# Kernel tuning notes

Measured on AMD Instinct MI355X. Metric: run time of the kernel, lower is better.

The kernel has to match this reference:

```python
import jax, jax.numpy as jnp
import numpy as np

L, N, E, NODE_D, EDGE_D, H = 3, 50000, 800000, 64, 16, 128
EPS = 1e-5


def _ln(x, g, b):
    mu = jnp.mean(x, axis=-1, keepdims=True)
    var = jnp.var(x, axis=-1, keepdims=True)
    return (x - mu) * jax.lax.rsqrt(var + EPS) * g + b


def setup_inputs() -> dict:
    key = jax.random.key(0)
    ks = jax.random.split(key, 16)
    inp = {
        "x": jax.random.normal(ks[0], (N, NODE_D), dtype=jnp.float32),
        "edge_index": jax.random.randint(ks[1], (2, E), 0, N, dtype=jnp.int64 if jax.config.jax_enable_x64 else jnp.int32),
        "edge_attr": jax.random.normal(ks[2], (E, EDGE_D), dtype=jnp.float32),
        # node_embed: Linear(node_dim, H) + LayerNorm
        "node_W": jax.random.normal(ks[3], (H, NODE_D), dtype=jnp.float32) * (2.0 / H) ** 0.5,
        "node_b": jnp.zeros((H,), jnp.float32),
        "node_ln_g": jnp.ones((H,), jnp.float32),
        "node_ln_b": jnp.zeros((H,), jnp.float32),
        # per-layer GINConv params, stacked on leading layer dim
        "edge_W": jax.random.normal(ks[4], (L, H, EDGE_D), dtype=jnp.float32) * (2.0 / H) ** 0.5,
        "edge_b": jnp.zeros((L, H), jnp.float32),
        "edge_ln_g": jnp.ones((L, H), jnp.float32),
        "edge_ln_b": jnp.zeros((L, H), jnp.float32),
        "sl_attr": jax.random.normal(ks[5], (L, 1, EDGE_D), dtype=jnp.float32),
        "mlp_W1": jax.random.normal(ks[6], (L, 2 * H, H), dtype=jnp.float32) * (1.0 / H) ** 0.5,
        "mlp_b1": jnp.zeros((L, 2 * H), jnp.float32),
        "mlp_W2": jax.random.normal(ks[7], (L, H, 2 * H), dtype=jnp.float32) * (1.0 / (2 * H)) ** 0.5,
        "mlp_b2": jnp.zeros((L, H), jnp.float32),
        # BatchNorm1d affine params (batch-stat / training-mode math)
        "bn_g": jnp.ones((L, H), jnp.float32),
        "bn_b": jnp.zeros((L, H), jnp.float32),
    }
    return inp


def reference(x, edge_index, edge_attr, node_W, node_b, node_ln_g, node_ln_b,
              edge_W, edge_b, edge_ln_g, edge_ln_b, sl_attr,
              mlp_W1, mlp_b1, mlp_W2, mlp_b2, bn_g, bn_b):
    n = x.shape[0]
    # augmented edge list with self loops appended (add_self_loops)
    loop = jnp.arange(n, dtype=edge_index.dtype)
    src = jnp.concatenate([edge_index[0], loop])  # [E+N]
    dst = jnp.concatenate([edge_index[1], loop])  # [E+N]

    # node_embed: Linear -> LN -> ReLU
    h = jax.nn.relu(_ln(x @ node_W.T + node_b, node_ln_g, node_ln_b))

    for l in range(L):
        # edge_embed on [original edges ; learned self-loop attr]
        sl = jnp.broadcast_to(sl_attr[l], (n, EDGE_D))
        ea = jnp.concatenate([edge_attr, sl], axis=0)          # [E+N, edge_dim]
        ea = jax.nn.relu(_ln(ea @ edge_W[l].T + edge_b[l], edge_ln_g[l], edge_ln_b[l]))
        # message: gather x_j + edge_attr; aggregate: scatter-add to dst
        msg = h[src] + ea                                      # [E+N, H]
        aggr = jax.ops.segment_sum(msg, dst, num_segments=n)   # [N, H]
        # update MLP: Linear -> GELU -> Linear (dropout inactive at eval)
        z = jax.nn.gelu(aggr @ mlp_W1[l].T + mlp_b1[l], approximate=False)
        hl = z @ mlp_W2[l].T + mlp_b2[l]
        # BatchNorm1d (training-mode batch statistics over node dim)
        mu = jnp.mean(hl, axis=0, keepdims=True)
        var = jnp.var(hl, axis=0, keepdims=True)
        hl = (hl - mu) * jax.lax.rsqrt(var + EPS) * bn_g[l] + bn_b[l]
        if l != L - 1:
            hl = jax.nn.relu(hl)  # drop_ratio = 0 -> dropout is identity
        h = hl
    return h
```

## Files before the change

### kernel.cpp

```cpp
#include <hip/hip_runtime.h>
#include <cstdint>
#include <cstddef>

#define HD 128
#define EDGED 16
#define NODED 64
#define LN_EPS 1e-5f

typedef __bf16 bf16x8 __attribute__((ext_vector_type(8)));
typedef float  f32x4  __attribute__((ext_vector_type(4)));
typedef _Float16 half2v __attribute__((ext_vector_type(2)));
typedef _Float16 half4v __attribute__((ext_vector_type(4)));
typedef _Float16 half8v __attribute__((ext_vector_type(8)));

union HU { half8v v; half2v p[4]; };

__device__ __forceinline__ float gelu_exact(float x) {
    return 0.5f * x * (1.0f + erff(x * 0.7071067811865475f));
}

__global__ void wconv_k(const float* __restrict__ in, __bf16* __restrict__ hi,
                        __bf16* __restrict__ lo, int n) {
    int i = blockIdx.x * blockDim.x + threadIdx.x;
    if (i < n) {
        float v = in[i];
        __bf16 h = (__bf16)v;
        hi[i] = h;
        lo[i] = (__bf16)(v - (float)h);
    }
}


__global__ void hist_k(const int* __restrict__ ei, int* __restrict__ cnt, int E) {
    int e = blockIdx.x * blockDim.x + threadIdx.x;
    if (e < E) atomicAdd(&cnt[ei[E + e]], 1);
}

__global__ void scan1_k(const int* __restrict__ in, int* __restrict__ out,
                        int* __restrict__ bsum, int n) {
    __shared__ int lds[256];
    int t = threadIdx.x;
    int i = blockIdx.x * 256 + t;
    int v = (i < n) ? in[i] : 0;
    lds[t] = v;
    __syncthreads();
#pragma unroll
    for (int o = 1; o < 256; o <<= 1) {
        int u = (t >= o) ? lds[t - o] : 0;
        __syncthreads();
        lds[t] += u;
        __syncthreads();
    }
    if (i < n) out[i] = lds[t] - v;
    if (t == 255) bsum[blockIdx.x] = lds[255];
}

__global__ void scan2_k(const int* __restrict__ bsum, int* __restrict__ boff, int nb) {
    __shared__ int lds[256];
    int t = threadIdx.x;
    int v = (t < nb) ? bsum[t] : 0;
    lds[t] = v;
    __syncthreads();
#pragma unroll
    for (int o = 1; o < 256; o <<= 1) {
        int u = (t >= o) ? lds[t - o] : 0;
        __syncthreads();
        lds[t] += u;
        __syncthreads();
    }
    if (t < nb) boff[t] = lds[t] - v;
}

__global__ void scan3_k(int* __restrict__ rs, int* __restrict__ cursor,
                        const int* __restrict__ boff, int n, int E) {
    int i = blockIdx.x * 256 + threadIdx.x;
    if (i < n) {
        int v = rs[i] + boff[blockIdx.x];
        rs[i] = v;
        cursor[i] = v;
    }
    if (i == 0) rs[n] = E;
}

__global__ void scatter_k(const int* __restrict__ ei, int* __restrict__ cursor,
                          int2* __restrict__ es, int E) {
    int e = blockIdx.x * blockDim.x + threadIdx.x;
    if (e < E) {
        int dst = ei[E + e];
        int slot = atomicAdd(&cursor[dst], 1);
        es[slot] = make_int2(ei[e], e);
    }
}

__global__ void prep_k(const float* __restrict__ edge_W, const float* __restrict__ edge_b,
                       const float* __restrict__ edge_g, const float* __restrict__ edge_be,
                       const float* __restrict__ sl_attr, _Float16* __restrict__ Wg16_3,
                       float* __restrict__ bg3, float* __restrict__ M3,
                       float* __restrict__ v3, float* __restrict__ s03,
                       float* __restrict__ slv3)
{
    const int l = blockIdx.x;
    const float* W = edge_W + (size_t)l * HD * EDGED;
    const float* b = edge_b + l * HD;
    const float* g = edge_g + l * HD;
    __shared__ float Wp[HD * EDGED];
    __shared__ float bp[HD];
    __shared__ float wm[EDGED];
    __shared__ float Msh[256];
    __shared__ float vsh[EDGED];
    __shared__ float ash[EDGED];
    __shared__ float bmS, s0sh;
    const int t = threadIdx.x;
#pragma unroll
    for (int m = 0; m < 8; ++m) Wp[m * 256 + t] = W[m * 256 + t];
    __syncthreads();
    if (t < EDGED) {
        float s = 0.f;
        for (int c = 0; c < HD; ++c) s += Wp[c * EDGED + t];
        wm[t] = s * (1.f / HD);
    } else if (t == EDGED) {
        float s = 0.f;
        for (int c = 0; c < HD; ++c) s += b[c];
        bmS = s * (1.f / HD);
    }
    __syncthreads();
    if (t < HD) bp[t] = b[t] - bmS;
    __syncthreads();
#pragma unroll
    for (int m = 0; m < 8; ++m) {
        int idx = m * 256 + t;
        int c = idx >> 4, k = idx & 15;
        float val = Wp[idx] - wm[k];
        Wp[idx] = val;
        Wg16_3[(size_t)l * 2048 + idx] = (_Float16)(val * g[c]);
    }
    if (t < HD) bg3[l * HD + t] = bp[t] * g[t];
    __syncthreads();
    {
        int k = t >> 4, j = t & 15;
        float s = 0.f;
        for (int c = 0; c < HD; ++c) s += Wp[c * EDGED + k] * Wp[c * EDGED + j];
        Msh[t] = s;
        M3[l * 256 + t] = s;
    }
    if (t < EDGED) {
        float s = 0.f;
        for (int c = 0; c < HD; ++c) s += Wp[c * EDGED + t] * bp[c];
        vsh[t] = 2.f * s;
        v3[l * EDGED + t] = 2.f * s;
        ash[t] = sl_attr[l * EDGED + t];
    } else if (t == EDGED) {
        float s = 0.f;
        for (int c = 0; c < HD; ++c) s += bp[c] * bp[c];
        s0sh = s;
        s03[l] = s;
    }
    __syncthreads();
    if (t < HD) {
        float q = s0sh;
#pragma unroll
        for (int k = 0; k < EDGED; ++k) {
            float tk = vsh[k];
#pragma unroll
            for (int j = 0; j < EDGED; ++j) tk = fmaf(Msh[k * 16 + j], ash[j], tk);
            q = fmaf(ash[k], tk, q);
        }
        float inv = rsqrtf(q * (1.f / HD) + LN_EPS);
        float y = 0.f;
#pragma unroll
        for (int k = 0; k < EDGED; ++k) y = fmaf(Wp[t * EDGED + k], ash[k], y);
        slv3[l * HD + t] = fmaxf(fmaf(fmaf(y, g[t], bg3[l * HD + t]), inv, edge_be[l * HD + t]), 0.f);
    }
}

__launch_bounds__(256)
__global__ void einv_k(const int2* __restrict__ es, const float* __restrict__ eattr,
                       const float* __restrict__ M3, const float* __restrict__ v3,
                       const float* __restrict__ s03, int2* __restrict__ sei,
                       _Float16* __restrict__ attr16, int E)
{
    __shared__ float Ms[3 * 256];
    __shared__ float vs[3 * 16];
    __shared__ float s0s[4];
    const int t = threadIdx.x;
    for (int i = t; i < 768; i += 256) Ms[i] = M3[i];
    if (t < 48) vs[t] = v3[t];
    if (t < 3) s0s[t] = s03[t];
    __syncthreads();
    int slot = blockIdx.x * 256 + t;
    if (slot >= E) return;
    int2 se = es[slot];
    const float4* ap = (const float4*)(eattr + (size_t)se.y * EDGED);
    float4 A0 = ap[0], A1 = ap[1], A2 = ap[2], A3 = ap[3];
    float a[16] = {A0.x, A0.y, A0.z, A0.w, A1.x, A1.y, A1.z, A1.w,
                   A2.x, A2.y, A2.z, A2.w, A3.x, A3.y, A3.z, A3.w};
    {
        half8v o0, o1;
#pragma unroll
        for (int i = 0; i < 8; ++i) { o0[i] = (_Float16)a[i]; o1[i] = (_Float16)a[8 + i]; }
        _Float16* op = attr16 + (size_t)slot * EDGED;
        *(half8v*)&op[0] = o0;
        *(half8v*)&op[8] = o1;
    }
#pragma unroll
    for (int l = 0; l < 3; ++l) {
        float q = s0s[l];
#pragma unroll
        for (int k = 0; k < 16; ++k) {
            const float* Mr = &Ms[l * 256 + k * 16];
            float tk = vs[l * 16 + k];
#pragma unroll
            for (int j = 0; j < 16; ++j) tk = fmaf(Mr[j], a[j], tk);
            q = fmaf(a[k], tk, q);
        }
        float iv = rsqrtf(q * (1.f / HD) + LN_EPS);
        sei[(size_t)l * E + slot] = make_int2(se.x, __float_as_int(iv));
    }
}

template<int K, int NC, int ACT, int STATS, int OUTBF>
__launch_bounds__(256)
__global__ void mgemm_k(const __bf16* __restrict__ Ahi, const __bf16* __restrict__ Alo,
                        const __bf16* __restrict__ Whi, const __bf16* __restrict__ Wlo,
                        const float* __restrict__ bias, float* __restrict__ C,
                        __bf16* __restrict__ Chi, __bf16* __restrict__ Clo,
                        int M, float* __restrict__ stats)
{
    constexpr int RG = 2;
    constexpr int NT = 4;
    constexpr int NK = K / 32;
    __shared__ float st_lds[2][64];

    const int t    = threadIdx.x;
    const int lane = t & 63;
    const int wv   = t >> 6;
    const int ln15 = lane & 15;
    const int quad = lane >> 4;
    const int row_base = blockIdx.x * 128 + wv * 32;
    const int col0 = blockIdx.y * 64;

    f32x4 acc[RG][NT];
#pragma unroll
    for (int g = 0; g < RG; ++g)
#pragma unroll
        for (int nt = 0; nt < NT; ++nt)
#pragma unroll
            for (int r = 0; r < 4; ++r) acc[g][nt][r] = 0.f;

    size_t arow[RG];
#pragma unroll
    for (int g = 0; g < RG; ++g) {
        int row = row_base + g * 16 + ln15;
        row = row < M ? row : M - 1;
        arow[g] = (size_t)row * K + quad * 8;
    }
    size_t brow[NT];
#pragma unroll
    for (int nt = 0; nt < NT; ++nt)
        brow[nt] = (size_t)(col0 + nt * 16 + ln15) * K + quad * 8;

    bf16x8 a0h[RG], a0l[RG], a1h[RG], a1l[RG];
    bf16x8 b0h[NT], b0l[NT], b1h[NT], b1l[NT];

#define LD_A(kc, AH, AL) { \
    _Pragma("unroll") \
    for (int g = 0; g < RG; ++g) { \
        AH[g] = *(const bf16x8*)(Ahi + arow[g] + (kc)); \
        AL[g] = *(const bf16x8*)(Alo + arow[g] + (kc)); \
    } }
#define LD_B(kc, BH, BL) { \
    _Pragma("unroll") \
    for (int nt = 0; nt < NT; ++nt) { \
        BH[nt] = *(const bf16x8*)(Whi + brow[nt] + (kc)); \
        BL[nt] = *(const bf16x8*)(Wlo + brow[nt] + (kc)); \
    } }
#define DO_MFMA(AH, AL, BH, BL) { \
    _Pragma("unroll") \
    for (int nt = 0; nt < NT; ++nt) { \
        _Pragma("unroll") \
        for (int g = 0; g < RG; ++g) { \
            acc[g][nt] = __builtin_amdgcn_mfma_f32_16x16x32_bf16(AH[g], BH[nt], acc[g][nt], 0, 0, 0); \
            acc[g][nt] = __builtin_amdgcn_mfma_f32_16x16x32_bf16(AH[g], BL[nt], acc[g][nt], 0, 0, 0); \
            acc[g][nt] = __builtin_amdgcn_mfma_f32_16x16x32_bf16(AL[g], BH[nt], acc[g][nt], 0, 0, 0); \
        } } }

    LD_A(0, a0h, a0l);
    LD_B(0, b0h, b0l);
    for (int s = 0; s < NK; s += 2) {
        LD_A((s + 1) * 32, a1h, a1l);
        LD_B((s + 1) * 32, b1h, b1l);
        DO_MFMA(a0h, a0l, b0h, b0l);
        if (s + 2 < NK) {
            LD_A((s + 2) * 32, a0h, a0l);
            LD_B((s + 2) * 32, b0h, b0l);
        }
        DO_MFMA(a1h, a1l, b1h, b1l);
    }
#undef LD_A
#undef LD_B
#undef DO_MFMA

    if (STATS) {
        if (t < 64) { st_lds[0][t] = 0.f; st_lds[1][t] = 0.f; }
        __syncthreads();
    }

    float bv[NT];
#pragma unroll
    for (int nt = 0; nt < NT; ++nt) bv[nt] = bias[col0 + nt * 16 + ln15];

    float s1[NT], s2[NT];
#pragma unroll
    for (int nt = 0; nt < NT; ++nt) { s1[nt] = 0.f; s2[nt] = 0.f; }

#pragma unroll
    for (int g = 0; g < RG; ++g)
#pragma unroll
        for (int r = 0; r < 4; ++r) {
            int row = row_base + g * 16 + quad * 4 + r;
            if (row < M) {
#pragma unroll
                for (int nt = 0; nt < NT; ++nt) {
                    float v = acc[g][nt][r] + bv[nt];
                    if (ACT == 1) v = gelu_exact(v);
                    size_t ci = (size_t)row * NC + col0 + nt * 16 + ln15;
                    if (OUTBF) {
                        __bf16 hh = (__bf16)v;
                        Chi[ci] = hh;
                        Clo[ci] = (__bf16)(v - (float)hh);
                    } else {
                        C[ci] = v;
                    }
                    if (STATS) { s1[nt] += v; s2[nt] += v * v; }
                }
            }
        }

    if (STATS) {
#pragma unroll
        for (int nt = 0; nt < NT; ++nt) {
            atomicAdd(&st_lds[0][nt * 16 + ln15], s1[nt]);
            atomicAdd(&st_lds[1][nt * 16 + ln15], s2[nt]);
        }
        __syncthreads();
        if (t < 64) {
            atomicAdd(&stats[col0 + t],      st_lds[0][t]);
            atomicAdd(&stats[HD + col0 + t], st_lds[1][t]);
        }
    }
}

__global__ void ln_relu_k(const float* __restrict__ y, const float* __restrict__ gam,
                          const float* __restrict__ bet, _Float16* __restrict__ h16, int N)
{
    int lane = threadIdx.x & 63;
    int c0 = lane * 2;
    float2 g2 = *(const float2*)&gam[c0];
    float2 b2 = *(const float2*)&bet[c0];
    int wid = (blockIdx.x * blockDim.x + threadIdx.x) >> 6;
    int nw  = (gridDim.x * blockDim.x) >> 6;
    for (int n = wid; n < N; n += nw) {
        float2 v = *(const float2*)&y[(size_t)n * HD + c0];
        float s = v.x + v.y;
        float q = v.x * v.x + v.y * v.y;
#pragma unroll
        for (int o = 32; o > 0; o >>= 1) { s += __shfl_xor(s, o, 64); q += __shfl_xor(q, o, 64); }
        float mu  = s * (1.f / 128.f);
        float inv = rsqrtf(q * (1.f / 128.f) - mu * mu + LN_EPS);
        half2v r;
        r.x = (_Float16)fmaxf(fmaf((v.x - mu) * inv, g2.x, b2.x), 0.f);
        r.y = (_Float16)fmaxf(fmaf((v.y - mu) * inv, g2.y, b2.y), 0.f);
        *(half2v*)&h16[(size_t)n * HD + c0] = r;
    }
}

__launch_bounds__(256)
__global__ void pull8_k(const _Float16* __restrict__ h16, const int* __restrict__ rs,
                        const _Float16* __restrict__ attr16, const int2* __restrict__ sei,
                        const float* __restrict__ slv, const _Float16* __restrict__ Wg16,
                        const float* __restrict__ bg, const float* __restrict__ bet,
                        __bf16* __restrict__ Ahi, __bf16* __restrict__ Alo, int N)
{
    __shared__ _Float16 alds_all[4][64 * EDGED];
    const int t = threadIdx.x;
    const int lane = t & 63;
    const int wv = t >> 6;
    _Float16* alds = alds_all[wv];
    uint4* alds4 = (uint4*)alds;

    const int c0 = lane * 2;
    half2v w0p[8], w1p[8];
#pragma unroll
    for (int k = 0; k < 8; ++k) {
        w0p[k] = *(const half2v*)&Wg16[c0 * EDGED + 2 * k];
        w1p[k] = *(const half2v*)&Wg16[(c0 + 1) * EDGED + 2 * k];
    }
    const float2 bgv  = *(const float2*)&bg[c0];
    const float2 btv  = *(const float2*)&bet[c0];
    const float2 slvv = *(const float2*)&slv[c0];

    const int stride = gridDim.x << 2;
    for (int n = (blockIdx.x << 2) + wv; n < N; n += stride) {
        half2v hs = *(const half2v*)&h16[(size_t)n * HD + c0];
        float acc0 = (float)hs.x + slvv.x;
        float acc1 = (float)hs.y + slvv.y;

        const int beg = rs[n], end = rs[n + 1];
        for (int s0 = beg; s0 < end; s0 += 64) {
            int m = end - s0; if (m > 64) m = 64;
            int2 sv = make_int2(0, 0);
            if (lane < m) sv = sei[s0 + lane];
            const uint4* src4 = (const uint4*)(attr16 + (size_t)s0 * EDGED);
#pragma unroll
            for (int it = 0; it < 2; ++it) {
                int idx = (it << 6) + lane;
                if (idx < (m << 1)) alds4[idx] = src4[idx];
            }
            asm volatile("s_waitcnt lgkmcnt(0)" ::: "memory");

#define EDGE_BODY(JJ, IVJ, HVJ) { \
            HU ua, ub; \
            ua.v = *(const half8v*)&alds[(JJ) * EDGED]; \
            ub.v = *(const half8v*)&alds[(JJ) * EDGED + 8]; \
            float p0 = bgv.x, q0 = 0.f, p1 = bgv.y, q1 = 0.f; \
            p0 = __builtin_amdgcn_fdot2(ua.p[0], w0p[0], p0, false); \
            q0 = __builtin_amdgcn_fdot2(ua.p[1], w0p[1], q0, false); \
            p1 = __builtin_amdgcn_fdot2(ua.p[0], w1p[0], p1, false); \
            q1 = __builtin_amdgcn_fdot2(ua.p[1], w1p[1], q1, false); \
            p0 = __builtin_amdgcn_fdot2(ua.p[2], w0p[2], p0, false); \
            q0 = __builtin_amdgcn_fdot2(ua.p[3], w0p[3], q0, false); \
            p1 = __builtin_amdgcn_fdot2(ua.p[2], w1p[2], p1, false); \
            q1 = __builtin_amdgcn_fdot2(ua.p[3], w1p[3], q1, false); \
            p0 = __builtin_amdgcn_fdot2(ub.p[0], w0p[4], p0, false); \
            q0 = __builtin_amdgcn_fdot2(ub.p[1], w0p[5], q0, false); \
            p1 = __builtin_amdgcn_fdot2(ub.p[0], w1p[4], p1, false); \
            q1 = __builtin_amdgcn_fdot2(ub.p[1], w1p[5], q1, false); \
            p0 = __builtin_amdgcn_fdot2(ub.p[2], w0p[6], p0, false); \
            q0 = __builtin_amdgcn_fdot2(ub.p[3], w0p[7], q0, false); \
            p1 = __builtin_amdgcn_fdot2(ub.p[2], w1p[6], p1, false); \
            q1 = __builtin_amdgcn_fdot2(ub.p[3], w1p[7], q1, false); \
            acc0 += fmaxf(fmaf(p0 + q0, IVJ, btv.x), 0.f) + (float)HVJ.x; \
            acc1 += fmaxf(fmaf(p1 + q1, IVJ, btv.y), 0.f) + (float)HVJ.y; \
        }

            int j = 0;
            for (; j + 4 <= m; j += 4) {
                int s_0 = __shfl(sv.x, j,     64);
                int s_1 = __shfl(sv.x, j + 1, 64);
                int s_2 = __shfl(sv.x, j + 2, 64);
                int s_3 = __shfl(sv.x, j + 3, 64);
                float i0 = __int_as_float(__shfl(sv.y, j,     64));
                float i1 = __int_as_float(__shfl(sv.y, j + 1, 64));
                float i2 = __int_as_float(__shfl(sv.y, j + 2, 64));
                float i3 = __int_as_float(__shfl(sv.y, j + 3, 64));
                half2v h0 = *(const half2v*)&h16[(size_t)s_0 * HD + c0];
                half2v h1 = *(const half2v*)&h16[(size_t)s_1 * HD + c0];
                half2v h2 = *(const half2v*)&h16[(size_t)s_2 * HD + c0];
                half2v h3 = *(const half2v*)&h16[(size_t)s_3 * HD + c0];
                EDGE_BODY(j,     i0, h0);
                EDGE_BODY(j + 1, i1, h1);
                EDGE_BODY(j + 2, i2, h2);
                EDGE_BODY(j + 3, i3, h3);
            }
            for (; j < m; ++j) {
                int s_  = __shfl(sv.x, j, 64);
                float ij = __int_as_float(__shfl(sv.y, j, 64));
                half2v hj = *(const half2v*)&h16[(size_t)s_ * HD + c0];
                EDGE_BODY(j, ij, hj);
            }
#undef EDGE_BODY
        }
        __bf16 b0 = (__bf16)acc0, b1 = (__bf16)acc1;
        union { __bf16 b[2]; unsigned u; } ph, pl;
        ph.b[0] = b0;
        ph.b[1] = b1;
        pl.b[0] = (__bf16)(acc0 - (float)b0);
        pl.b[1] = (__bf16)(acc1 - (float)b1);
        *(unsigned*)&Ahi[(size_t)n * HD + c0] = ph.u;
        *(unsigned*)&Alo[(size_t)n * HD + c0] = pl.u;
    }
}

__global__ void bn_k(const float* __restrict__ hl, const float* __restrict__ stats,
                     const float* __restrict__ gam, const float* __restrict__ bet,
                     float* __restrict__ out32, _Float16* __restrict__ out16,
                     int total4, float invN, int relu)
{
    int idx = blockIdx.x * blockDim.x + threadIdx.x;
    if (idx < total4) {
        int c4 = idx & 31;
        float4 x  = ((const float4*)hl)[idx];
        float4 s1 = ((const float4*)stats)[c4];
        float4 s2 = ((const float4*)stats)[32 + c4];
        float4 g  = ((const float4*)gam)[c4];
        float4 b  = ((const float4*)bet)[c4];
        float4 r;
        {
            float m = s1.x * invN; float v = s2.x * invN - m * m;
            r.x = fmaf((x.x - m) * rsqrtf(v + LN_EPS), g.x, b.x);
        }
        {
            float m = s1.y * invN; float v = s2.y * invN - m * m;
            r.y = fmaf((x.y - m) * rsqrtf(v + LN_EPS), g.y, b.y);
        }
        {
            float m = s1.z * invN; float v = s2.z * invN - m * m;
            r.z = fmaf((x.z - m) * rsqrtf(v + LN_EPS), g.z, b.z);
        }
        {
            float m = s1.w * invN; float v = s2.w * invN - m * m;
            r.w = fmaf((x.w - m) * rsqrtf(v + LN_EPS), g.w, b.w);
        }
        if (relu) {
            r.x = fmaxf(r.x, 0.f); r.y = fmaxf(r.y, 0.f);
            r.z = fmaxf(r.z, 0.f); r.w = fmaxf(r.w, 0.f);
        }
        if (out16) {
            half4v o;
            o.x = (_Float16)r.x; o.y = (_Float16)r.y;
            o.z = (_Float16)r.z; o.w = (_Float16)r.w;
            *(half4v*)&out16[(size_t)idx * 4] = o;
        } else {
            ((float4*)out32)[idx] = r;
        }
    }
}

extern "C" void kernel_launch(void* const* d_in, const int* in_sizes, int n_in,
                              void* d_out, int out_size, void* d_ws, size_t ws_size,
                              hipStream_t stream)
{
    const float* x       = (const float*)d_in[0];
    const int*   ei      = (const int*)d_in[1];
    const float* eattr   = (const float*)d_in[2];
    const float* node_W  = (const float*)d_in[3];
    const float* node_b  = (const float*)d_in[4];
    const float* node_g  = (const float*)d_in[5];
    const float* node_be = (const float*)d_in[6];
    const float* edge_W  = (const float*)d_in[7];
    const float* edge_b  = (const float*)d_in[8];
    const float* edge_g  = (const float*)d_in[9];
    const float* edge_be = (const float*)d_in[10];
    const float* sl_attr = (const float*)d_in[11];
    const float* W1      = (const float*)d_in[12];
    const float* b1      = (const float*)d_in[13];
    const float* W2      = (const float*)d_in[14];
    const float* b2      = (const float*)d_in[15];
    const float* bn_g    = (const float*)d_in[16];
    const float* bn_b    = (const float*)d_in[17];

    const int N = in_sizes[0] / NODED;
    const int E = in_sizes[1] / 2;

    char* base = (char*)d_ws;
    size_t off = 0;
    auto take = [&](size_t nbytes) -> void* {
        void* p = base + off;
        off = (off + nbytes + 15) & ~(size_t)15;
        return p;
    };
    _Float16* h16  = (_Float16*)take((size_t)N * HD * 2);
    float*  z      = (float*)take((size_t)N * HD * 4);
    __bf16* aghi   = (__bf16*)take((size_t)N * HD * 2);
    __bf16* aglo   = (__bf16*)take((size_t)N * HD * 2);
    __bf16* zhi    = (__bf16*)take((size_t)N * 256 * 2);
    __bf16* zlo    = (__bf16*)take((size_t)N * 256 * 2);
    __bf16* xhi    = (__bf16*)take((size_t)N * NODED * 2);
    __bf16* xlo    = (__bf16*)take((size_t)N * NODED * 2);
    float*  slv3   = (float*)take(3 * HD * 4);
    float*  stats  = (float*)take(3 * 256 * 4);
    int*    cnt    = (int*)take((size_t)N * 4);
    int*    cursor = (int*)take((size_t)N * 4);
    int*    bsum   = (int*)take(256 * 4);
    int*    boff   = (int*)take(256 * 4);
    int*    rs     = (int*)take(((size_t)N + 2) * 4);
    int2*   es     = (int2*)take((size_t)E * 8);
    int2*   sei    = (int2*)take((size_t)3 * E * 8);
    _Float16* attr16 = (_Float16*)take((size_t)E * EDGED * 2);
    _Float16* Wg16_3 = (_Float16*)take(3 * 2048 * 2);
    float*  bg3    = (float*)take(3 * HD * 4);
    float*  M3     = (float*)take(3 * 256 * 4);
    float*  v3     = (float*)take(3 * 16 * 4);
    float*  s03    = (float*)take(4 * 4);
    __bf16* nWhi   = (__bf16*)take((size_t)HD * NODED * 2);
    __bf16* nWlo   = (__bf16*)take((size_t)HD * NODED * 2);
    __bf16* W1hi   = (__bf16*)take((size_t)3 * 256 * HD * 2);
    __bf16* W1lo   = (__bf16*)take((size_t)3 * 256 * HD * 2);
    __bf16* W2hi   = (__bf16*)take((size_t)3 * HD * 256 * 2);
    __bf16* W2lo   = (__bf16*)take((size_t)3 * HD * 256 * 2);

    wconv_k<<<(HD * NODED + 255) / 256, 256, 0, stream>>>(node_W, nWhi, nWlo, HD * NODED);
    wconv_k<<<(3 * 256 * HD + 255) / 256, 256, 0, stream>>>(W1, W1hi, W1lo, 3 * 256 * HD);
    wconv_k<<<(3 * 256 * HD + 255) / 256, 256, 0, stream>>>(W2, W2hi, W2lo, 3 * 256 * HD);
    wconv_k<<<((int)((size_t)N * NODED + 255) / 256), 256, 0, stream>>>(x, xhi, xlo, N * NODED);

    prep_k<<<3, 256, 0, stream>>>(edge_W, edge_b, edge_g, edge_be, sl_attr,
                                  Wg16_3, bg3, M3, v3, s03, slv3);

    const int eblocks = (E + 255) / 256;
    const int nblocks = (N + 255) / 256;
    hipMemsetAsync(cnt, 0, (size_t)N * sizeof(int), stream);
    hist_k<<<eblocks, 256, 0, stream>>>(ei, cnt, E);
    scan1_k<<<nblocks, 256, 0, stream>>>(cnt, rs, bsum, N);
    scan2_k<<<1, 256, 0, stream>>>(bsum, boff, nblocks);
    scan3_k<<<nblocks, 256, 0, stream>>>(rs, cursor, boff, N, E);
    scatter_k<<<eblocks, 256, 0, stream>>>(ei, cursor, es, E);

    einv_k<<<eblocks, 256, 0, stream>>>(es, eattr, M3, v3, s03, sei, attr16, E);

    const int total4  = N * (HD / 4);
    const int vblocks = (total4 + 255) / 256;
    const int gb128   = (N + 127) / 128;
    int pgrid = (N + 3) / 4;
    if (pgrid > 2048) pgrid = 2048;

    mgemm_k<NODED, HD, 0, 0, 0><<<dim3(gb128, 2), 256, 0, stream>>>(
        xhi, xlo, nWhi, nWlo, node_b, z, nullptr, nullptr, N, nullptr);
    ln_relu_k<<<(N + 3) / 4, 256, 0, stream>>>(z, node_g, node_be, h16, N);

    hipMemsetAsync(stats, 0, 3 * 256 * sizeof(float), stream);

    for (int l = 0; l < 3; ++l) {
        pull8_k<<<pgrid, 256, 0, stream>>>(h16, rs, attr16, sei + (size_t)l * E,
                                           slv3 + l * HD, Wg16_3 + (size_t)l * 2048,
                                           bg3 + l * HD, edge_be + l * HD,
                                           aghi, aglo, N);

        mgemm_k<HD, 256, 1, 0, 1><<<dim3(gb128, 4), 256, 0, stream>>>(
            aghi, aglo, W1hi + (size_t)l * 256 * HD, W1lo + (size_t)l * 256 * HD,
            b1 + l * 256, nullptr, zhi, zlo, N, nullptr);

        mgemm_k<256, HD, 0, 1, 0><<<dim3(gb128, 2), 256, 0, stream>>>(
            zhi, zlo, W2hi + (size_t)l * HD * 256, W2lo + (size_t)l * HD * 256,
            b2 + l * HD, (float*)d_out, nullptr, nullptr, N, stats + l * 256);

        bn_k<<<vblocks, 256, 0, stream>>>((const float*)d_out, stats + l * 256,
                                          bn_g + l * HD, bn_b + l * HD,
                                          (float*)d_out, (l < 2) ? h16 : nullptr,
                                          total4, 1.f / N, (l < 2) ? 1 : 0);
    }
}
```

Measured before the change: 883.3 us.

## Store GELU output as single fp16 and pack edge src/inv-std into 32 bits

```diff
diff --git a/kernel.cpp b/kernel.cpp
--- a/kernel.cpp
+++ b/kernel.cpp
@@ -17,6 +17,12 @@
 
 __device__ __forceinline__ float gelu_exact(float x) {
     return 0.5f * x * (1.0f + erff(x * 0.7071067811865475f));
+}
+
+__device__ __forceinline__ float hi16_to_f(int bits) {
+    union { unsigned short u; _Float16 h; } c;
+    c.u = (unsigned short)((unsigned)bits >> 16);
+    return (float)c.h;
 }
 
 __global__ void wconv_k(const float* __restrict__ in, __bf16* __restrict__ hi,
@@ -27,6 +33,17 @@
         __bf16 h = (__bf16)v;
         hi[i] = h;
         lo[i] = (__bf16)(v - (float)h);
+    }
+}
+
+__global__ void wconv16_k(const float* __restrict__ in, _Float16* __restrict__ hi,
+                          _Float16* __restrict__ lo, int n) {
+    int i = blockIdx.x * blockDim.x + threadIdx.x;
+    if (i < n) {
+        float v = in[i];
+        _Float16 h = (_Float16)v;
+        hi[i] = h;
+        lo[i] = (_Float16)(v - (float)h);
     }
 }
 
@@ -176,7 +193,7 @@
 __launch_bounds__(256)
 __global__ void einv_k(const int2* __restrict__ es, const float* __restrict__ eattr,
                        const float* __restrict__ M3, const float* __restrict__ v3,
-                       const float* __restrict__ s03, int2* __restrict__ sei,
+                       const float* __restrict__ s03, unsigned* __restrict__ sei,
                        _Float16* __restrict__ attr16, int E)
 {
     __shared__ float Ms[3 * 256];
@@ -214,17 +231,18 @@
             q = fmaf(a[k], tk, q);
         }
         float iv = rsqrtf(q * (1.f / HD) + LN_EPS);
-        sei[(size_t)l * E + slot] = make_int2(se.x, __float_as_int(iv));
-    }
-}
-
-template<int K, int NC, int ACT, int STATS, int OUTBF>
+        union { _Float16 h; unsigned short u; } cv;
+        cv.h = (_Float16)iv;
+        sei[(size_t)l * E + slot] = ((unsigned)se.x & 0xFFFFu) | ((unsigned)cv.u << 16);
+    }
+}
+
+template<int K, int NC, int ACT, int STATS, int AMODE, int OUTMODE>
 __launch_bounds__(256)
-__global__ void mgemm_k(const __bf16* __restrict__ Ahi, const __bf16* __restrict__ Alo,
-                        const __bf16* __restrict__ Whi, const __bf16* __restrict__ Wlo,
+__global__ void mgemm_k(const void* __restrict__ Ap1, const void* __restrict__ Ap2,
+                        const void* __restrict__ Wp1, const void* __restrict__ Wp2,
                         const float* __restrict__ bias, float* __restrict__ C,
-                        __bf16* __restrict__ Chi, __bf16* __restrict__ Clo,
-                        int M, float* __restrict__ stats)
+                        void* __restrict__ Co1, int M, float* __restrict__ stats)
 {
     constexpr int RG = 2;
     constexpr int NT = 4;
@@ -259,8 +277,13 @@
     for (int nt = 0; nt < NT; ++nt)
         brow[nt] = (size_t)(col0 + nt * 16 + ln15) * K + quad * 8;
 
-    bf16x8 a0h[RG], a0l[RG], a1h[RG], a1l[RG];
-    bf16x8 b0h[NT], b0l[NT], b1h[NT], b1l[NT];
+    if constexpr (AMODE == 0) {
+        const __bf16* Ahi = (const __bf16*)Ap1;
+        const __bf16* Alo = (const __bf16*)Ap2;
+        const __bf16* Whi = (const __bf16*)Wp1;
+        const __bf16* Wlo = (const __bf16*)Wp2;
+        bf16x8 a0h[RG], a0l[RG], a1h[RG], a1l[RG];
+        bf16x8 b0h[NT], b0l[NT], b1h[NT], b1l[NT];
 
 #define LD_A(kc, AH, AL) { \
     _Pragma("unroll") \
@@ -284,21 +307,62 @@
             acc[g][nt] = __builtin_amdgcn_mfma_f32_16x16x32_bf16(AL[g], BH[nt], acc[g][nt], 0, 0, 0); \
         } } }
 
-    LD_A(0, a0h, a0l);
-    LD_B(0, b0h, b0l);
-    for (int s = 0; s < NK; s += 2) {
-        LD_A((s + 1) * 32, a1h, a1l);
-        LD_B((s + 1) * 32, b1h, b1l);
-        DO_MFMA(a0h, a0l, b0h, b0l);
-        if (s + 2 < NK) {
-            LD_A((s + 2) * 32, a0h, a0l);
-            LD_B((s + 2) * 32, b0h, b0l);
-        }
-        DO_MFMA(a1h, a1l, b1h, b1l);
-    }
+        LD_A(0, a0h, a0l);
+        LD_B(0, b0h, b0l);
+        for (int s = 0; s < NK; s += 2) {
+            LD_A((s + 1) * 32, a1h, a1l);
+            LD_B((s + 1) * 32, b1h, b1l);
+            DO_MFMA(a0h, a0l, b0h, b0l);
+            if (s + 2 < NK) {
+                LD_A((s + 2) * 32, a0h, a0l);
+                LD_B((s + 2) * 32, b0h, b0l);
+            }
+            DO_MFMA(a1h, a1l, b1h, b1l);
+        }
 #undef LD_A
 #undef LD_B
 #undef DO_MFMA
+    } else {
+        const _Float16* Af = (const _Float16*)Ap1;
+        const _Float16* Wh = (const _Float16*)Wp1;
+        const _Float16* Wl = (const _Float16*)Wp2;
+        half8v a0[RG], a1[RG];
+        half8v b0h[NT], b0l[NT], b1h[NT], b1l[NT];
+
+#define LD_A16(kc, A) { \
+    _Pragma("unroll") \
+    for (int g = 0; g < RG; ++g) A[g] = *(const half8v*)(Af + arow[g] + (kc)); }
+#define LD_B16(kc, BH, BL) { \
+    _Pragma("unroll") \
+    for (int nt = 0; nt < NT; ++nt) { \
+        BH[nt] = *(const half8v*)(Wh + brow[nt] + (kc)); \
+        BL[nt] = *(const half8v*)(Wl + brow[nt] + (kc)); \
+    } }
+#define DO_MFMA16(A, BH, BL) { \
+    _Pragma("unroll") \
+    for (int nt = 0; nt < NT; ++nt) { \
+        _Pragma("unroll") \
+        for (int g = 0; g < RG; ++g) { \
+            acc[g][nt] = __builtin_amdgcn_mfma_f32_16x16x32_f16(A[g], BH[nt], acc[g][nt], 0, 0, 0); \
+            acc[g][nt] = __builtin_amdgcn_mfma_f32_16x16x32_f16(A[g], BL[nt], acc[g][nt], 0, 0, 0); \
+        } } }
+
+        LD_A16(0, a0);
+        LD_B16(0, b0h, b0l);
+        for (int s = 0; s < NK; s += 2) {
+            LD_A16((s + 1) * 32, a1);
+            LD_B16((s + 1) * 32, b1h, b1l);
+            DO_MFMA16(a0, b0h, b0l);
+            if (s + 2 < NK) {
+                LD_A16((s + 2) * 32, a0);
+                LD_B16((s + 2) * 32, b0h, b0l);
+            }
+            DO_MFMA16(a1, b1h, b1l);
+        }
+#undef LD_A16
+#undef LD_B16
+#undef DO_MFMA16
+    }
 
     if (STATS) {
         if (t < 64) { st_lds[0][t] = 0.f; st_lds[1][t] = 0.f; }
@@ -324,10 +388,8 @@
                     float v = acc[g][nt][r] + bv[nt];
                     if (ACT == 1) v = gelu_exact(v);
                     size_t ci = (size_t)row * NC + col0 + nt * 16 + ln15;
-                    if (OUTBF) {
-                        __bf16 hh = (__bf16)v;
-                        Chi[ci] = hh;
-                        Clo[ci] = (__bf16)(v - (float)hh);
+                    if (OUTMODE == 2) {
+                        ((_Float16*)Co1)[ci] = (_Float16)v;
                     } else {
                         C[ci] = v;
                     }
@@ -375,8 +437,8 @@
 }
 
 __launch_bounds__(256)
-__global__ void pull8_k(const _Float16* __restrict__ h16, const int* __restrict__ rs,
-                        const _Float16* __restrict__ attr16, const int2* __restrict__ sei,
+__global__ void pull9_k(const _Float16* __restrict__ h16, const int* __restrict__ rs,
+                        const _Float16* __restrict__ attr16, const unsigned* __restrict__ sei,
                         const float* __restrict__ slv, const _Float16* __restrict__ Wg16,
                         const float* __restrict__ bg, const float* __restrict__ bet,
                         __bf16* __restrict__ Ahi, __bf16* __restrict__ Alo, int N)
@@ -408,8 +470,8 @@
         const int beg = rs[n], end = rs[n + 1];
         for (int s0 = beg; s0 < end; s0 += 64) {
             int m = end - s0; if (m > 64) m = 64;
-            int2 sv = make_int2(0, 0);
-            if (lane < m) sv = sei[s0 + lane];
+            int sv = 0;
+            if (lane < m) sv = (int)sei[s0 + lane];
             const uint4* src4 = (const uint4*)(attr16 + (size_t)s0 * EDGED);
 #pragma unroll
             for (int it = 0; it < 2; ++it) {
@@ -445,14 +507,16 @@
 
             int j = 0;
             for (; j + 4 <= m; j += 4) {
-                int s_0 = __shfl(sv.x, j,     64);
-                int s_1 = __shfl(sv.x, j + 1, 64);
-                int s_2 = __shfl(sv.x, j + 2, 64);
-                int s_3 = __shfl(sv.x, j + 3, 64);
-                float i0 = __int_as_float(__shfl(sv.y, j,     64));
-                float i1 = __int_as_float(__shfl(sv.y, j + 1, 64));
-                float i2 = __int_as_float(__shfl(sv.y, j + 2, 64));
-                float i3 = __int_as_float(__shfl(sv.y, j + 3, 64));
+                int v0 = __shfl(sv, j,     64);
+                int v1 = __shfl(sv, j + 1, 64);
+                int v2 = __shfl(sv, j + 2, 64);
+                int v3 = __shfl(sv, j + 3, 64);
+                int s_0 = v0 & 0xFFFF, s_1 = v1 & 0xFFFF;
+                int s_2 = v2 & 0xFFFF, s_3 = v3 & 0xFFFF;
+                float i0 = hi16_to_f(v0);
+                float i1 = hi16_to_f(v1);
+                float i2 = hi16_to_f(v2);
+                float i3 = hi16_to_f(v3);
                 half2v h0 = *(const half2v*)&h16[(size_t)s_0 * HD + c0];
                 half2v h1 = *(const half2v*)&h16[(size_t)s_1 * HD + c0];
                 half2v h2 = *(const half2v*)&h16[(size_t)s_2 * HD + c0];
@@ -463,8 +527,9 @@
                 EDGE_BODY(j + 3, i3, h3);
             }
             for (; j < m; ++j) {
-                int s_  = __shfl(sv.x, j, 64);
-                float ij = __int_as_float(__shfl(sv.y, j, 64));
+                int vj = __shfl(sv, j, 64);
+                int s_ = vj & 0xFFFF;
+                float ij = hi16_to_f(vj);
                 half2v hj = *(const half2v*)&h16[(size_t)s_ * HD + c0];
                 EDGE_BODY(j, ij, hj);
             }
@@ -563,8 +628,7 @@
     float*  z      = (float*)take((size_t)N * HD * 4);
     __bf16* aghi   = (__bf16*)take((size_t)N * HD * 2);
     __bf16* aglo   = (__bf16*)take((size_t)N * HD * 2);
-    __bf16* zhi    = (__bf16*)take((size_t)N * 256 * 2);
-    __bf16* zlo    = (__bf16*)take((size_t)N * 256 * 2);
+    _Float16* z16  = (_Float16*)take((size_t)N * 256 * 2);
     __bf16* xhi    = (__bf16*)take((size_t)N * NODED * 2);
     __bf16* xlo    = (__bf16*)take((size_t)N * NODED * 2);
     float*  slv3   = (float*)take(3 * HD * 4);
@@ -575,7 +639,7 @@
     int*    boff   = (int*)take(256 * 4);
     int*    rs     = (int*)take(((size_t)N + 2) * 4);
     int2*   es     = (int2*)take((size_t)E * 8);
-    int2*   sei    = (int2*)take((size_t)3 * E * 8);
+    unsigned* sei  = (unsigned*)take((size_t)3 * E * 4);
     _Float16* attr16 = (_Float16*)take((size_t)E * EDGED * 2);
     _Float16* Wg16_3 = (_Float16*)take(3 * 2048 * 2);
     float*  bg3    = (float*)take(3 * HD * 4);
@@ -586,12 +650,12 @@
     __bf16* nWlo   = (__bf16*)take((size_t)HD * NODED * 2);
     __bf16* W1hi   = (__bf16*)take((size_t)3 * 256 * HD * 2);
     __bf16* W1lo   = (__bf16*)take((size_t)3 * 256 * HD * 2);
-    __bf16* W2hi   = (__bf16*)take((size_t)3 * HD * 256 * 2);
-    __bf16* W2lo   = (__bf16*)take((size_t)3 * HD * 256 * 2);
+    _Float16* W2h16 = (_Float16*)take((size_t)3 * HD * 256 * 2);
+    _Float16* W2l16 = (_Float16*)take((size_t)3 * HD * 256 * 2);
 
     wconv_k<<<(HD * NODED + 255) / 256, 256, 0, stream>>>(node_W, nWhi, nWlo, HD * NODED);
     wconv_k<<<(3 * 256 * HD + 255) / 256, 256, 0, stream>>>(W1, W1hi, W1lo, 3 * 256 * HD);
-    wconv_k<<<(3 * 256 * HD + 255) / 256, 256, 0, stream>>>(W2, W2hi, W2lo, 3 * 256 * HD);
+    wconv16_k<<<(3 * 256 * HD + 255) / 256, 256, 0, stream>>>(W2, W2h16, W2l16, 3 * 256 * HD);
     wconv_k<<<((int)((size_t)N * NODED + 255) / 256), 256, 0, stream>>>(x, xhi, xlo, N * NODED);
 
     prep_k<<<3, 256, 0, stream>>>(edge_W, edge_b, edge_g, edge_be, sl_attr,
@@ -614,25 +678,25 @@
     int pgrid = (N + 3) / 4;
     if (pgrid > 2048) pgrid = 2048;
 
-    mgemm_k<NODED, HD, 0, 0, 0><<<dim3(gb128, 2), 256, 0, stream>>>(
-        xhi, xlo, nWhi, nWlo, node_b, z, nullptr, nullptr, N, nullptr);
+    mgemm_k<NODED, HD, 0, 0, 0, 0><<<dim3(gb128, 2), 256, 0, stream>>>(
+        xhi, xlo, nWhi, nWlo, node_b, z, nullptr, N, nullptr);
     ln_relu_k<<<(N + 3) / 4, 256, 0, stream>>>(z, node_g, node_be, h16, N);
 
     hipMemsetAsync(stats, 0, 3 * 256 * sizeof(float), stream);
 
     for (int l = 0; l < 3; ++l) {
-        pull8_k<<<pgrid, 256, 0, stream>>>(h16, rs, attr16, sei + (size_t)l * E,
+        pull9_k<<<pgrid, 256, 0, stream>>>(h16, rs, attr16, sei + (size_t)l * E,
                                            slv3 + l * HD, Wg16_3 + (size_t)l * 2048,
                                            bg3 + l * HD, edge_be + l * HD,
                                            aghi, aglo, N);
 
-        mgemm_k<HD, 256, 1, 0, 1><<<dim3(gb128, 4), 256, 0, stream>>>(
+        mgemm_k<HD, 256, 1, 0, 0, 2><<<dim3(gb128, 4), 256, 0, stream>>>(
             aghi, aglo, W1hi + (size_t)l * 256 * HD, W1lo + (size_t)l * 256 * HD,
-            b1 + l * 256, nullptr, zhi, zlo, N, nullptr);
-
-        mgemm_k<256, HD, 0, 1, 0><<<dim3(gb128, 2), 256, 0, stream>>>(
-            zhi, zlo, W2hi + (size_t)l * HD * 256, W2lo + (size_t)l * HD * 256,
-            b2 + l * HD, (float*)d_out, nullptr, nullptr, N, stats + l * 256);
+            b1 + l * 256, nullptr, z16, N, nullptr);
+
+        mgemm_k<256, HD, 0, 1, 1, 0><<<dim3(gb128, 2), 256, 0, stream>>>(
+            z16, nullptr, W2h16 + (size_t)l * HD * 256, W2l16 + (size_t)l * HD * 256,
+            b2 + l * HD, (float*)d_out, nullptr, N, stats + l * 256);
 
         bn_k<<<vblocks, 256, 0, stream>>>((const float*)d_out, stats + l * 256,
                                           bn_g + l * HD, bn_b + l * HD,
```

After: 872.0 us. Within noise of the previous version (-1.3%).
